# Performance work log

Hardware: AMD Instinct MI355X
Metric: run time of the kernel (lower is better)

Reference implementation:

```python
import jax, jax.numpy as jnp
import numpy as np

N = 100000   # nodes
E = 1200000  # edges
FIN = 128    # in_channels
H = 64       # hidden_channels
OUT = 1      # out_channels


def setup_inputs() -> dict:
    key = jax.random.key(0)
    ks = jax.random.split(key, 12)
    s = 0.05
    return {
        "x": jax.random.normal(ks[0], (N, FIN), jnp.float32),
        "edge_index": jax.random.randint(ks[1], (2, E), 0, N, dtype=jnp.int64),
        "W0": jax.random.normal(ks[2], (FIN, H), jnp.float32) * s,
        "b0": jnp.zeros((H,), jnp.float32),
        "W1": jax.random.normal(ks[3], (H, H), jnp.float32) * s,
        "b1": jnp.zeros((H,), jnp.float32),
        "W2": jax.random.normal(ks[4], (H, OUT), jnp.float32) * s,
        "b2": jnp.zeros((OUT,), jnp.float32),
        "Wm1": jax.random.normal(ks[5], (OUT, H), jnp.float32) * s,
        "bm1": jnp.zeros((H,), jnp.float32),
        "Wm2": jax.random.normal(ks[6], (H, OUT), jnp.float32) * s,
        "bm2": jnp.zeros((OUT,), jnp.float32),
    }


def reference(x, edge_index, W0, b0, W1, b1, W2, b2, Wm1, bm1, Wm2, bm2):
    # GCNConv (PyG default): add self-loops, symmetric normalization D^-1/2 A D^-1/2
    loop = jnp.arange(N, dtype=edge_index.dtype)
    src = jnp.concatenate([edge_index[0], loop])  # [E+N]
    dst = jnp.concatenate([edge_index[1], loop])
    deg = jax.ops.segment_sum(jnp.ones(E + N, jnp.float32), dst, num_segments=N)
    dinv = jax.lax.rsqrt(deg)  # deg >= 1 thanks to self-loops
    norm = dinv[src] * dinv[dst]  # [E+N]

    def conv(h, W, b):
        h = h @ W  # [N, d_out]
        msg = h[src] * norm[:, None]  # gather + scale, [E+N, d_out]
        return jax.ops.segment_sum(msg, dst, num_segments=N) + b

    h = jax.nn.relu(conv(x, W0, b0))   # input layer (dropout is identity in eval)
    h = jax.nn.relu(conv(h, W1, b1))   # hidden layer
    h = conv(h, W2, b2)                # output GCN layer -> [N, OUT]
    # MLP head
    h = jax.nn.relu(h @ Wm1 + bm1) @ Wm2 + bm2
    return h
```

## Files before the change

kernel.cpp:

```cpp
#include <hip/hip_runtime.h>
#include <hip/hip_fp16.h>
#include <math.h>

#define ELL_CAP 48
#define NBUCK 391
#define SLB 256
#define SLICE 48

typedef _Float16 half8 __attribute__((ext_vector_type(8)));
typedef float floatx4 __attribute__((ext_vector_type(4)));


__device__ __forceinline__ __half2 u2h(unsigned u) {
  __half2 h; __builtin_memcpy(&h, &u, 4); return h;
}
__device__ __forceinline__ unsigned h2u(__half2 h) {
  unsigned u; __builtin_memcpy(&u, &h, 4); return u;
}


__global__ __launch_bounds__(1024) void k_bucket(const int* __restrict__ src,
                                                 const int* __restrict__ dst,
                                                 int* __restrict__ hist_g,
                                                 int* __restrict__ buckets, int E) {
  __shared__ int histL[NBUCK];
  const int tid = threadIdx.x, b = blockIdx.x;
  for (int i = tid; i < NBUCK; i += 1024) histL[i] = 0;
  __syncthreads();

  const long s0 = (long)b * E / SLB, s1 = (long)(b + 1) * E / SLB;
  for (long e = s0 + tid; e < s1; e += 1024) {
    int s = src[e], d = dst[e];
    int bi = d >> 8;
    int pos = atomicAdd(&histL[bi], 1);
    if (pos < SLICE)
      buckets[(long)bi * (SLB * SLICE) + b * SLICE + pos] = ((d & 255) << 24) | s;
  }
  __syncthreads();

  for (int i = tid; i < NBUCK; i += 1024) hist_g[i * SLB + b] = min(histL[i], SLICE);
}


__global__ __launch_bounds__(512) void k_ellbuild(const int* __restrict__ buckets,
                                                  const int* __restrict__ hist_g,
                                                  int* __restrict__ cnt,
                                                  int* __restrict__ ell,
                                                  float* __restrict__ dinv, int n) {
  __shared__ int cnt_l[256];
  __shared__ int ell_l[256 * ELL_CAP];
  __shared__ int cslice[SLB];
  __shared__ unsigned char lim4[256];
  const int b = blockIdx.x, tid = threadIdx.x;
  if (tid < 256) cnt_l[tid] = 0;
  if (tid < SLB) cslice[tid] = hist_g[b * SLB + tid];
  __syncthreads();

  const int s = tid >> 1;
  const int m = cslice[s];
  const int4* bk4 = (const int4*)(buckets + (long)b * (SLB * SLICE) + s * SLICE);
  const int nq = (m + 3) >> 2;
  for (int j = (tid & 1); j < nq; j += 2) {
    int4 q = bk4[j];
    const int e0 = j * 4;
    int v[4] = {q.x, q.y, q.z, q.w};
#pragma unroll
    for (int k = 0; k < 4; ++k) {
      if (e0 + k < m) {
        int p = v[k];
        int ld = ((unsigned)p) >> 24;
        int pos = atomicAdd(&cnt_l[ld], 1);
        if (pos < ELL_CAP) ell_l[ld * ELL_CAP + pos] = p & 0xFFFFFF;
      }
    }
  }
  __syncthreads();

  const int d0 = b << 8;
  const int node = d0 + tid;
  const int rows = min(256, n - d0);
  if (tid < rows) {
    int c = cnt_l[tid];
    if (c > ELL_CAP) c = ELL_CAP;
    cnt[node] = c;
    dinv[node] = 1.0f / sqrtf((float)(c + 1));
    lim4[tid] = (unsigned char)((c + 3) >> 2);
  }
  __syncthreads();

  int4* dst4 = (int4*)(ell + (long)d0 * ELL_CAP);
  const int4* src4 = (const int4*)ell_l;
  const int tot = rows * 12;
  for (int i = tid; i < tot; i += 512) {
    int r = i / 12, w = i - r * 12;
    if (w < (int)lim4[r]) dst4[i] = src4[i];
  }
}


__global__ __launch_bounds__(256) void k_gemm_mfma128(const float* __restrict__ Xf,
                                                      const float* __restrict__ W,
                                                      const float* __restrict__ dinv,
                                                      __half* __restrict__ out,
                                                      __half* __restrict__ zrowA,
                                                      __half* __restrict__ zrowB, int n) {
  constexpr int K = 128, SP = K + 8, NS = K / 32;
  __shared__ __half Wl[64 * SP];
  const int tx = threadIdx.x;

  if (blockIdx.x == 0 && tx < 64) { zrowA[tx] = __float2half(0.f); zrowB[tx] = __float2half(0.f); }

  for (int idx = tx; idx < (K / 2) * 64; idx += 256) {
    int k2 = idx >> 6, col = idx & 63;
    __half2 h = __floats2half2_rn(W[(2 * k2) * 64 + col], W[(2 * k2 + 1) * 64 + col]);
    *(__half2*)&Wl[col * SP + 2 * k2] = h;
  }
  __syncthreads();

  const int lane = tx & 63;
  const int l15 = lane & 15;
  const int quad = lane >> 4;
  const long base = (long)blockIdx.x * 64 + (tx >> 6) * 16;

  long arow = base + l15;
  if (arow >= n) arow = n - 1;

  half8 afrag[NS];
#pragma unroll
  for (int s = 0; s < NS; ++s) {
    float4 lo = *(const float4*)&Xf[arow * K + s * 32 + quad * 8];
    float4 hi = *(const float4*)&Xf[arow * K + s * 32 + quad * 8 + 4];
    half8 a;
    a[0] = (_Float16)lo.x; a[1] = (_Float16)lo.y;
    a[2] = (_Float16)lo.z; a[3] = (_Float16)lo.w;
    a[4] = (_Float16)hi.x; a[5] = (_Float16)hi.y;
    a[6] = (_Float16)hi.z; a[7] = (_Float16)hi.w;
    afrag[s] = a;
  }

  floatx4 acc[4];
#pragma unroll
  for (int t = 0; t < 4; ++t) acc[t] = (floatx4){0.f, 0.f, 0.f, 0.f};

#pragma unroll
  for (int s = 0; s < NS; ++s) {
#pragma unroll
    for (int t = 0; t < 4; ++t) {
      half8 bfrag = *(const half8*)&Wl[(t * 16 + l15) * SP + s * 32 + quad * 8];
      acc[t] = __builtin_amdgcn_mfma_f32_16x16x32_f16(afrag[s], bfrag, acc[t], 0, 0, 0);
    }
  }

#pragma unroll
  for (int r = 0; r < 4; ++r) {
    long node = base + quad * 4 + r;
    if (node < n) {
      float dv = dinv[node];
#pragma unroll
      for (int t = 0; t < 4; ++t)
        out[node * 64 + t * 16 + l15] = __float2half(acc[t][r] * dv);
    }
  }
}


template <typename EPI>
__device__ __forceinline__ void gather8_one(int grp, const __half* __restrict__ hs,
                                            const int* __restrict__ ell,
                                            const int* __restrict__ cnt,
                                            const float* __restrict__ dinv,
                                            int n, int lane, EPI epi) {
  const int l8 = lane & 7;
  const int node = grp * 8 + (lane >> 3);
  const bool alive = node < n;
  const int nd = alive ? node : 0;
  const int c = alive ? cnt[nd] : 0;
  const float di = alive ? dinv[nd] : 0.f;
  const int* row = &ell[(long)nd * ELL_CAP];

  int s0 = (l8 < c) ? row[l8] : n;
  int s1 = (8 + l8 < c) ? row[8 + l8] : n;
  int s2 = (16 + l8 < c) ? row[16 + l8] : n;

  int cm = c;
  cm = max(cm, __shfl_xor(cm, 8, 64));
  cm = max(cm, __shfl_xor(cm, 16, 64));
  cm = max(cm, __shfl_xor(cm, 32, 64));
  const int nph = (cm + 7) >> 3;

  float accf[8];
  {
    float4 v = alive ? *(const float4*)&hs[(long)nd * 64 + l8 * 8]
                     : make_float4(0.f, 0.f, 0.f, 0.f);
    const unsigned* up = (const unsigned*)&v;
#pragma unroll
    for (int t = 0; t < 4; ++t) {
      float2 f = __half22float2(u2h(up[t]));
      accf[2 * t] = f.x; accf[2 * t + 1] = f.y;
    }
  }

  auto phase = [&](int reg) {
    int ss[8];
#pragma unroll
    for (int u = 0; u < 8; ++u) ss[u] = __shfl(reg, u, 8);
    float4 vv[8];
#pragma unroll
    for (int u = 0; u < 8; ++u) vv[u] = *(const float4*)&hs[(long)ss[u] * 64 + l8 * 8];
#pragma unroll
    for (int u = 0; u < 8; ++u) {
      const unsigned* up = (const unsigned*)&vv[u];
#pragma unroll
      for (int t = 0; t < 4; ++t) {
        float2 f = __half22float2(u2h(up[t]));
        accf[2 * t] += f.x; accf[2 * t + 1] += f.y;
      }
    }
  };

  if (nph > 0) phase(s0);
  if (nph > 1) phase(s1);
  if (nph > 2) phase(s2);
  for (int ph = 3; ph < nph; ++ph) {
    int reg = (ph * 8 + l8 < c) ? row[ph * 8 + l8] : n;
    phase(reg);
  }

  epi(accf, di, nd, l8, alive);
}


__global__ __launch_bounds__(256) void k_gather_gemm(const __half* __restrict__ hs0,
                                                     const int* __restrict__ ell,
                                                     const int* __restrict__ cnt,
                                                     const float* __restrict__ dinv,
                                                     const float* __restrict__ b0,
                                                     const float* __restrict__ W1,
                                                     __half* __restrict__ hs1, int n) {
  constexpr int SP = 72;
  __shared__ __half Wl[64 * SP];
  __shared__ __half As[64 * SP];
  const int tx = threadIdx.x;
  const int lane = tx & 63;
  const int w = tx >> 6;
  const long blockBase = (long)blockIdx.x * 64;

  for (int idx = tx; idx < 32 * 64; idx += 256) {
    int k2 = idx >> 6, col = idx & 63;
    __half2 h = __floats2half2_rn(W1[(2 * k2) * 64 + col], W1[(2 * k2 + 1) * 64 + col]);
    *(__half2*)&Wl[col * SP + 2 * k2] = h;
  }

#pragma unroll
  for (int p = 0; p < 2; ++p) {
    int g = blockIdx.x * 8 + w * 2 + p;
    gather8_one(g, hs0, ell, cnt, dinv, n, lane,
                [&](const float (&accf)[8], float di, int nd, int l8, bool alive) {
      if (!alive) return;
      int row = (int)(nd - blockBase);
      float4 bv0 = *(const float4*)&b0[l8 * 8];
      float4 bv1 = *(const float4*)&b0[l8 * 8 + 4];
      uint4 o;
      o.x = h2u(__floats2half2_rn(fmaxf(bv0.x + di * accf[0], 0.f),
                                  fmaxf(bv0.y + di * accf[1], 0.f)));
      o.y = h2u(__floats2half2_rn(fmaxf(bv0.z + di * accf[2], 0.f),
                                  fmaxf(bv0.w + di * accf[3], 0.f)));
      o.z = h2u(__floats2half2_rn(fmaxf(bv1.x + di * accf[4], 0.f),
                                  fmaxf(bv1.y + di * accf[5], 0.f)));
      o.w = h2u(__floats2half2_rn(fmaxf(bv1.z + di * accf[6], 0.f),
                                  fmaxf(bv1.w + di * accf[7], 0.f)));
      *(uint4*)&As[row * SP + l8 * 8] = o;
    });
  }
  __syncthreads();

  const int l15 = lane & 15;
  const int quad = lane >> 4;
  half8 afrag[2];
#pragma unroll
  for (int s = 0; s < 2; ++s)
    afrag[s] = *(const half8*)&As[(w * 16 + l15) * SP + s * 32 + quad * 8];

  floatx4 acc[4];
#pragma unroll
  for (int t = 0; t < 4; ++t) acc[t] = (floatx4){0.f, 0.f, 0.f, 0.f};
#pragma unroll
  for (int s = 0; s < 2; ++s) {
#pragma unroll
    for (int t = 0; t < 4; ++t) {
      half8 bfrag = *(const half8*)&Wl[(t * 16 + l15) * SP + s * 32 + quad * 8];
      acc[t] = __builtin_amdgcn_mfma_f32_16x16x32_f16(afrag[s], bfrag, acc[t], 0, 0, 0);
    }
  }

#pragma unroll
  for (int r = 0; r < 4; ++r) {
    long node = blockBase + w * 16 + quad * 4 + r;
    if (node < n) {
      float dv = dinv[node];
#pragma unroll
      for (int t = 0; t < 4; ++t)
        hs1[node * 64 + t * 16 + l15] = __float2half(acc[t][r] * dv);
    }
  }
}

__global__ __launch_bounds__(256) void k_gather64x8_dot(const __half* __restrict__ hs,
                                                        const int* __restrict__ ell,
                                                        const int* __restrict__ cnt,
                                                        const float* __restrict__ dinv,
                                                        const float* __restrict__ b1,
                                                        const float* __restrict__ W2,
                                                        float* __restrict__ h2s, int n) {
  if (blockIdx.x == 0 && threadIdx.x == 0) h2s[n] = 0.f;
  const int wave = (blockIdx.x * 256 + threadIdx.x) >> 6;
  gather8_one(wave, hs, ell, cnt, dinv, n, threadIdx.x & 63,
              [&](const float (&accf)[8], float di, int node, int l8, bool alive) {
    float4 bv0 = *(const float4*)&b1[l8 * 8];
    float4 bv1 = *(const float4*)&b1[l8 * 8 + 4];
    float4 wv0 = *(const float4*)&W2[l8 * 8];
    float4 wv1 = *(const float4*)&W2[l8 * 8 + 4];
    float part = fmaxf(bv0.x + di * accf[0], 0.f) * wv0.x;
    part = fmaf(fmaxf(bv0.y + di * accf[1], 0.f), wv0.y, part);
    part = fmaf(fmaxf(bv0.z + di * accf[2], 0.f), wv0.z, part);
    part = fmaf(fmaxf(bv0.w + di * accf[3], 0.f), wv0.w, part);
    part = fmaf(fmaxf(bv1.x + di * accf[4], 0.f), wv1.x, part);
    part = fmaf(fmaxf(bv1.y + di * accf[5], 0.f), wv1.y, part);
    part = fmaf(fmaxf(bv1.z + di * accf[6], 0.f), wv1.z, part);
    part = fmaf(fmaxf(bv1.w + di * accf[7], 0.f), wv1.w, part);
#pragma unroll
    for (int off = 1; off < 8; off <<= 1) part += __shfl_xor(part, off, 8);
    if (alive && l8 == 0) h2s[node] = di * part;
  });
}


__global__ __launch_bounds__(256) void k_gather1_mlp_x8(const float* __restrict__ h2s,
                                                        const int* __restrict__ ell,
                                                        const int* __restrict__ cnt,
                                                        const float* __restrict__ dinv,
                                                        const float* __restrict__ b2,
                                                        const float* __restrict__ Wm1,
                                                        const float* __restrict__ bm1,
                                                        const float* __restrict__ Wm2,
                                                        const float* __restrict__ bm2,
                                                        float* __restrict__ out, int n) {
  __shared__ float w1s[64], w2s[64], b1s[64];
  if (threadIdx.x < 64) {
    w1s[threadIdx.x] = Wm1[threadIdx.x];
    w2s[threadIdx.x] = Wm2[threadIdx.x];
    b1s[threadIdx.x] = bm1[threadIdx.x];
  }
  __syncthreads();
  const int tid = threadIdx.x;
  const int lane = tid & 63;
  const int l8 = lane & 7;
  const int wave = (blockIdx.x * 256 + tid) >> 6;
  const int node = wave * 8 + (lane >> 3);
  const bool alive = node < n;
  const int nd = alive ? node : 0;
  const int c = alive ? cnt[nd] : 0;
  const float di = alive ? dinv[nd] : 0.f;
  const int* row = &ell[(long)nd * ELL_CAP];

  int cm = c;
  cm = max(cm, __shfl_xor(cm, 8, 64));
  cm = max(cm, __shfl_xor(cm, 16, 64));
  cm = max(cm, __shfl_xor(cm, 32, 64));
  const int nph = (cm + 7) >> 3;

  float acc = (alive && l8 == 0) ? h2s[nd] : 0.f;
  for (int ph = 0; ph < nph; ++ph) {
    int j = ph * 8 + l8;
    int s = (j < c) ? row[j] : n;
    acc += h2s[s];
  }
#pragma unroll
  for (int off = 1; off < 8; off <<= 1) acc += __shfl_xor(acc, off, 8);

  const float sv = b2[0] + di * acc;
  float o = 0.f;
#pragma unroll
  for (int q = 0; q < 8; ++q) {
    int j = l8 * 8 + q;
    o = fmaf(fmaxf(fmaf(sv, w1s[j], b1s[j]), 0.f), w2s[j], o);
  }
#pragma unroll
  for (int off = 1; off < 8; off <<= 1) o += __shfl_xor(o, off, 8);
  if (alive && l8 == 0) out[nd] = o + bm2[0];
}


extern "C" void kernel_launch(void* const* d_in, const int* in_sizes, int n_in,
                              void* d_out, int out_size, void* d_ws, size_t ws_size,
                              hipStream_t stream) {
  const float* x   = (const float*)d_in[0];
  const int*   ei  = (const int*)d_in[1];
  const float* W0  = (const float*)d_in[2];
  const float* b0  = (const float*)d_in[3];
  const float* W1  = (const float*)d_in[4];
  const float* b1  = (const float*)d_in[5];
  const float* W2  = (const float*)d_in[6];
  const float* b2  = (const float*)d_in[7];
  const float* Wm1 = (const float*)d_in[8];
  const float* bm1 = (const float*)d_in[9];
  const float* Wm2 = (const float*)d_in[10];
  const float* bm2 = (const float*)d_in[11];

  const int n = in_sizes[0] / 128;
  const int E = in_sizes[1] / 2;
  const int* src = ei;
  const int* dst = ei + E;

  float*  ws   = (float*)d_ws;
  float*  dinv = ws;
  int*    cnt  = (int*)(ws + n);
  int*    ell  = cnt + n;
  __half* bufA = (__half*)(ell + (size_t)n * ELL_CAP);
  __half* bufB = bufA + (size_t)(n + 1) * 64;
  float*  h2s  = (float*)(bufB + (size_t)(n + 1) * 64);
  int*    hist_g = (int*)(h2s + (n + 1));
  int*    buckets = (int*)bufA;

  const int g8b = (((n + 7) / 8) + 3) / 4;
  const int mfb = (n + 63) / 64;

  k_bucket<<<SLB, 1024, 0, stream>>>(src, dst, hist_g, buckets, E);
  k_ellbuild<<<NBUCK, 512, 0, stream>>>(buckets, hist_g, cnt, ell, dinv, n);

  k_gemm_mfma128<<<mfb, 256, 0, stream>>>(x, W0, dinv, bufA,
                                          bufA + (size_t)n * 64,
                                          bufB + (size_t)n * 64, n);

  k_gather_gemm<<<mfb, 256, 0, stream>>>(bufA, ell, cnt, dinv, b0, W1, bufB, n);

  k_gather64x8_dot<<<g8b, 256, 0, stream>>>(bufB, ell, cnt, dinv, b1, W2, h2s, n);

  k_gather1_mlp_x8<<<g8b, 256, 0, stream>>>(h2s, ell, cnt, dinv, b2, Wm1, bm1,
                                            Wm2, bm2, (float*)d_out, n);
}
```

Baseline: 199.9 us.

## Replace two-pass bucketed ELL build with direct global-atomic scatter

Drops the shared-memory bucketing and ELL-build kernels and builds the ELL adjacency with one global atomicAdd per edge into per-node counters, after a zeroing kernel. The degree-normalisation dinv is now computed inside the first GEMM epilogue from the raw counts, and the gather kernels clamp counts to ELL_CAP. This removes a bucket round-trip through memory and one kernel's shared-memory staging, but adds contended random global atomics and scattered 4-byte writes. Because edges are inserted by atomic order, neighbour order varies from run to run.

New measurement: 260.0 us. 30.0% more time.

```diff
diff --git a/kernel.cpp b/kernel.cpp
--- a/kernel.cpp
+++ b/kernel.cpp
@@ -3,9 +3,6 @@
 #include <math.h>
 
 #define ELL_CAP 48
-#define NBUCK 391
-#define SLB 256
-#define SLICE 48
 
 typedef _Float16 half8 __attribute__((ext_vector_type(8)));
 typedef float floatx4 __attribute__((ext_vector_type(4)));
@@ -19,88 +16,29 @@
 }
 
 
-__global__ __launch_bounds__(1024) void k_bucket(const int* __restrict__ src,
-                                                 const int* __restrict__ dst,
-                                                 int* __restrict__ hist_g,
-                                                 int* __restrict__ buckets, int E) {
-  __shared__ int histL[NBUCK];
-  const int tid = threadIdx.x, b = blockIdx.x;
-  for (int i = tid; i < NBUCK; i += 1024) histL[i] = 0;
-  __syncthreads();
-
-  const long s0 = (long)b * E / SLB, s1 = (long)(b + 1) * E / SLB;
-  for (long e = s0 + tid; e < s1; e += 1024) {
-    int s = src[e], d = dst[e];
-    int bi = d >> 8;
-    int pos = atomicAdd(&histL[bi], 1);
-    if (pos < SLICE)
-      buckets[(long)bi * (SLB * SLICE) + b * SLICE + pos] = ((d & 255) << 24) | s;
-  }
-  __syncthreads();
-
-  for (int i = tid; i < NBUCK; i += 1024) hist_g[i * SLB + b] = min(histL[i], SLICE);
-}
-
-
-__global__ __launch_bounds__(512) void k_ellbuild(const int* __restrict__ buckets,
-                                                  const int* __restrict__ hist_g,
+__global__ __launch_bounds__(1024) void k_zero(int* __restrict__ cnt, int n) {
+  int i = blockIdx.x * 1024 + threadIdx.x;
+  if (i < n) cnt[i] = 0;
+}
+
+
+__global__ __launch_bounds__(1024) void k_scatter(const int* __restrict__ src,
+                                                  const int* __restrict__ dst,
                                                   int* __restrict__ cnt,
-                                                  int* __restrict__ ell,
-                                                  float* __restrict__ dinv, int n) {
-  __shared__ int cnt_l[256];
-  __shared__ int ell_l[256 * ELL_CAP];
-  __shared__ int cslice[SLB];
-  __shared__ unsigned char lim4[256];
-  const int b = blockIdx.x, tid = threadIdx.x;
-  if (tid < 256) cnt_l[tid] = 0;
-  if (tid < SLB) cslice[tid] = hist_g[b * SLB + tid];
-  __syncthreads();
-
-  const int s = tid >> 1;
-  const int m = cslice[s];
-  const int4* bk4 = (const int4*)(buckets + (long)b * (SLB * SLICE) + s * SLICE);
-  const int nq = (m + 3) >> 2;
-  for (int j = (tid & 1); j < nq; j += 2) {
-    int4 q = bk4[j];
-    const int e0 = j * 4;
-    int v[4] = {q.x, q.y, q.z, q.w};
-#pragma unroll
-    for (int k = 0; k < 4; ++k) {
-      if (e0 + k < m) {
-        int p = v[k];
-        int ld = ((unsigned)p) >> 24;
-        int pos = atomicAdd(&cnt_l[ld], 1);
-        if (pos < ELL_CAP) ell_l[ld * ELL_CAP + pos] = p & 0xFFFFFF;
-      }
-    }
-  }
-  __syncthreads();
-
-  const int d0 = b << 8;
-  const int node = d0 + tid;
-  const int rows = min(256, n - d0);
-  if (tid < rows) {
-    int c = cnt_l[tid];
-    if (c > ELL_CAP) c = ELL_CAP;
-    cnt[node] = c;
-    dinv[node] = 1.0f / sqrtf((float)(c + 1));
-    lim4[tid] = (unsigned char)((c + 3) >> 2);
-  }
-  __syncthreads();
-
-  int4* dst4 = (int4*)(ell + (long)d0 * ELL_CAP);
-  const int4* src4 = (const int4*)ell_l;
-  const int tot = rows * 12;
-  for (int i = tid; i < tot; i += 512) {
-    int r = i / 12, w = i - r * 12;
-    if (w < (int)lim4[r]) dst4[i] = src4[i];
+                                                  int* __restrict__ ell, int E) {
+  int i = blockIdx.x * 1024 + threadIdx.x;
+  if (i < E) {
+    int s = src[i], d = dst[i];
+    int pos = atomicAdd(&cnt[d], 1);
+    if (pos < ELL_CAP) ell[(long)d * ELL_CAP + pos] = s;
   }
 }
 
 
 __global__ __launch_bounds__(256) void k_gemm_mfma128(const float* __restrict__ Xf,
                                                       const float* __restrict__ W,
-                                                      const float* __restrict__ dinv,
+                                                      const int* __restrict__ cnt,
+                                                      float* __restrict__ dinv,
                                                       __half* __restrict__ out,
                                                       __half* __restrict__ zrowA,
                                                       __half* __restrict__ zrowB, int n) {
@@ -155,7 +93,8 @@
   for (int r = 0; r < 4; ++r) {
     long node = base + quad * 4 + r;
     if (node < n) {
-      float dv = dinv[node];
+      float dv = 1.0f / sqrtf((float)(cnt[node] + 1));
+      if (l15 == 0) dinv[node] = dv;
 #pragma unroll
       for (int t = 0; t < 4; ++t)
         out[node * 64 + t * 16 + l15] = __float2half(acc[t][r] * dv);
@@ -174,7 +113,7 @@
   const int node = grp * 8 + (lane >> 3);
   const bool alive = node < n;
   const int nd = alive ? node : 0;
-  const int c = alive ? cnt[nd] : 0;
+  const int c = alive ? min(cnt[nd], ELL_CAP) : 0;
   const float di = alive ? dinv[nd] : 0.f;
   const int* row = &ell[(long)nd * ELL_CAP];
 
@@ -359,7 +298,7 @@
   const int node = wave * 8 + (lane >> 3);
   const bool alive = node < n;
   const int nd = alive ? node : 0;
-  const int c = alive ? cnt[nd] : 0;
+  const int c = alive ? min(cnt[nd], ELL_CAP) : 0;
   const float di = alive ? dinv[nd] : 0.f;
   const int* row = &ell[(long)nd * ELL_CAP];
 
@@ -419,16 +358,14 @@
   __half* bufA = (__half*)(ell + (size_t)n * ELL_CAP);
   __half* bufB = bufA + (size_t)(n + 1) * 64;
   float*  h2s  = (float*)(bufB + (size_t)(n + 1) * 64);
-  int*    hist_g = (int*)(h2s + (n + 1));
-  int*    buckets = (int*)bufA;
 
   const int g8b = (((n + 7) / 8) + 3) / 4;
   const int mfb = (n + 63) / 64;
 
-  k_bucket<<<SLB, 1024, 0, stream>>>(src, dst, hist_g, buckets, E);
-  k_ellbuild<<<NBUCK, 512, 0, stream>>>(buckets, hist_g, cnt, ell, dinv, n);
-
-  k_gemm_mfma128<<<mfb, 256, 0, stream>>>(x, W0, dinv, bufA,
+  k_zero<<<(n + 1023) / 1024, 1024, 0, stream>>>(cnt, n);
+  k_scatter<<<(E + 1023) / 1024, 1024, 0, stream>>>(src, dst, cnt, ell, E);
+
+  k_gemm_mfma128<<<mfb, 256, 0, stream>>>(x, W0, cnt, dinv, bufA,
                                           bufA + (size_t)n * 64,
                                           bufB + (size_t)n * 64, n);
 
```
